# Kernel tuning notes

Measured on AMD Instinct MI355X. Metric: run time of the kernel, lower is better.

The kernel has to match this reference:

```python
import jax, jax.numpy as jnp
import numpy as np

B, N, C, E, K, L = 8, 20000, 256, 320000, 3, 2
EPS = 1e-5

def setup_inputs() -> dict:
    key = jax.random.key(0)
    ks = jax.random.split(key, 8)
    features = jax.random.normal(ks[0], (B * N, C), dtype=jnp.float32)
    edge_index = jax.random.randint(ks[1], (2, E), 0, N, dtype=jnp.int64)
    # ChebConv params per layer: K linear weights [C,C] (no per-lin bias) + one bias [C]
    W = jax.random.normal(ks[2], (L, K, C, C), dtype=jnp.float32) * 0.05
    b = jax.random.normal(ks[3], (L, C), dtype=jnp.float32) * 0.05
    # node-mode LayerNorm affine params per layer
    ln_w = jnp.ones((L, C), dtype=jnp.float32)
    ln_b = jnp.zeros((L, C), dtype=jnp.float32)
    return {"features": features, "W": W, "b": b, "ln_w": ln_w, "ln_b": ln_b,
            "edge_index": edge_index, "batch_size": B}


def reference(features, W, b, ln_w, ln_b, edge_index, batch_size):
    n = features.shape[0] // batch_size
    c = features.shape[-1]
    src, dst = edge_index[0], edge_index[1]
    # sym-normalized Laplacian, lambda_max=2: L_hat = 2L/lmax - I = -D^-1/2 A D^-1/2
    deg = jax.ops.segment_sum(jnp.ones_like(src, dtype=features.dtype), src, num_segments=n)
    dis = jnp.where(deg > 0, jax.lax.rsqrt(jnp.where(deg > 0, deg, 1.0)), 0.0)
    norm = -dis[src] * dis[dst]  # [E]
    n_layers, k_order = W.shape[0], W.shape[1]

    def prop(x):  # L_hat @ x via gather-scale-scatter
        return jax.ops.segment_sum(norm[:, None] * x[src], dst, num_segments=n)

    def cheb(x, Wl, bl):
        Tx0 = x
        out = Tx0 @ Wl[0]
        Tx1 = prop(Tx0)
        out = out + Tx1 @ Wl[1]
        for k in range(2, k_order):
            Tx2 = 2.0 * prop(Tx1) - Tx0
            out = out + Tx2 @ Wl[k]
            Tx0, Tx1 = Tx1, Tx2
        return out + bl

    def single(feats):  # [n, c] -> [n, c]
        x = feats
        for i in range(n_layers):
            # NOTE: module passes original features to every layer's conv (faithful)
            x = cheb(feats, W[i], b[i])
            mu = jnp.mean(x, axis=-1, keepdims=True)
            var = jnp.var(x, axis=-1, keepdims=True)
            x = (x - mu) * jax.lax.rsqrt(var + EPS) * ln_w[i] + ln_b[i]
            # dropout p=0.0 -> identity
        return x

    fb = features.reshape(batch_size, n, c)
    return jax.vmap(single)(fb)
```

## Files before the change

kernel.cpp:

```cpp
#include <hip/hip_runtime.h>
#include <stdint.h>

#define BB 8
#define NN 20000
#define CC 256
#define EE 320000
#define KK 3
#define MROWS (BB * NN)
#define ROWU (BB * CC)

__device__ __forceinline__ float bf2f(ushort u) {
    union { uint32_t ui; float f; } v; v.ui = ((uint32_t)u) << 16; return v.f;
}
__device__ __forceinline__ ushort f2bf(float f) {
    union { uint32_t ui; float f; } v; v.f = f;
    uint32_t r = (v.ui + 0x7FFFu + ((v.ui >> 16) & 1u)) >> 16;
    return (ushort)r;
}

typedef __bf16 bf16x8 __attribute__((ext_vector_type(8)));
typedef float  f32x4  __attribute__((ext_vector_type(4)));

__device__ __forceinline__ void gload16(const void* gptr, void* lptr) {
    __builtin_amdgcn_global_load_lds(
        (const __attribute__((address_space(1))) void*)gptr,
        (__attribute__((address_space(3))) void*)lptr, 16, 0, 0);
}

__global__ void detect_k(const int* __restrict__ raw, int* __restrict__ flag) {
    int i = blockIdx.x * 256 + threadIdx.x;
    int v = 0;
    int idx = 2 * i + 1;
    if (i < EE) v = raw[idx];
    unsigned long long m = __ballot(v != 0);
    if ((threadIdx.x & 63) == 0 && m) atomicOr(flag, 1);
}

__global__ void convert_k(const int* __restrict__ raw, const int* __restrict__ flag,
                          int* __restrict__ src, int* __restrict__ dst) {
    int e = blockIdx.x * 256 + threadIdx.x;
    if (e >= EE) return;
    if (*flag == 0) {
        src[e] = raw[2 * e];
        dst[e] = raw[2 * EE + 2 * e];
    } else {
        src[e] = raw[e];
        dst[e] = raw[EE + e];
    }
}

__global__ void count_k(const int* __restrict__ src, const int* __restrict__ dst,
                        int* __restrict__ deg_out, int* __restrict__ cnt_in) {
    int e = blockIdx.x * 256 + threadIdx.x;
    if (e >= EE) return;
    atomicAdd(&deg_out[src[e]], 1);
    atomicAdd(&cnt_in[dst[e]], 1);
}

__global__ void __launch_bounds__(1024) scan_k(const int* __restrict__ cnt_in,
                                               const int* __restrict__ deg_out,
                                               int* __restrict__ row_ptr,
                                               float* __restrict__ dis) {
    __shared__ int wpart[16];
    const int t = threadIdx.x;
    const int lane = t & 63, wid = t >> 6;
    const int base = t * 20;
    int local[20];
    int sum = 0;
#pragma unroll
    for (int i = 0; i < 20; i++) {
        int idx = base + i;
        int v = (idx < NN) ? cnt_in[idx] : 0;
        local[i] = sum;
        sum += v;
    }
    int sc = sum;
#pragma unroll
    for (int off = 1; off < 64; off <<= 1) {
        int u = __shfl_up(sc, off, 64);
        if (lane >= off) sc += u;
    }
    if (lane == 63) wpart[wid] = sc;
    __syncthreads();
    if (wid == 0 && lane < 16) {
        int v = wpart[lane];
#pragma unroll
        for (int off = 1; off < 16; off <<= 1) {
            int u = __shfl_up(v, off, 64);
            if (lane >= off) v += u;
        }
        wpart[lane] = v;
    }
    __syncthreads();
    int wbase = (wid > 0) ? wpart[wid - 1] : 0;
    int tbase = wbase + sc - sum;
#pragma unroll
    for (int i = 0; i < 20; i++) {
        int idx = base + i;
        if (idx < NN) row_ptr[idx] = tbase + local[i];
    }
    if (t == 1023) row_ptr[NN] = tbase + sum;
    for (int i = t; i < NN; i += 1024) {
        int d = deg_out[i];
        dis[i] = (d > 0) ? rsqrtf((float)d) : 0.0f;
    }
}

__global__ void fill_k(const int* __restrict__ src, const int* __restrict__ dst,
                       const int* __restrict__ row_ptr, int* __restrict__ fillc,
                       const float* __restrict__ dis,
                       int* __restrict__ col, float* __restrict__ w) {
    int e = blockIdx.x * 256 + threadIdx.x;
    if (e >= EE) return;
    int s = src[e], d = dst[e];
    int pos = row_ptr[d] + atomicAdd(&fillc[d], 1);
    col[pos] = s;
    w[pos] = -dis[s] * dis[d];
}

__global__ void cvt_k(const float* __restrict__ x, ushort* __restrict__ y) {
    size_t idx = ((size_t)blockIdx.x * 256 + threadIdx.x) * 4;
    int row = (int)(idx >> 8);
    int c = (int)(idx & 255);
    int b = row / NN, n = row - b * NN;
    float4 v = *(const float4*)(x + idx);
    ushort4 o = make_ushort4(f2bf(v.x), f2bf(v.y), f2bf(v.z), f2bf(v.w));
    *(ushort4*)(y + ((size_t)(n * BB + b) * CC + c)) = o;
}

__global__ void wprep_k(const float* __restrict__ W, ushort* __restrict__ wt) {
    int idx = blockIdx.x * 256 + threadIdx.x;
    if (idx >= 256 * 768) return;
    int n = idx / 768, k = idx % 768;
    int sel = k >> 8, kk = k & 255;
    const float* W1 = W + KK * CC * CC;
    float v;
    if (sel == 0)      v = W1[kk * CC + n] - W1[2 * CC * CC + kk * CC + n];
    else if (sel == 1) v = W1[CC * CC + kk * CC + n];
    else               v = 2.0f * W1[2 * CC * CC + kk * CC + n];
    wt[idx] = f2bf(v);
}

__global__ void __launch_bounds__(256) prop_k(const ushort* __restrict__ x,
                                              ushort* __restrict__ y,
                                              const int* __restrict__ row_ptr,
                                              const int* __restrict__ col,
                                              const float* __restrict__ w) {
    const int n = blockIdx.x;
    const int t = threadIdx.x;
    const int beg = row_ptr[n], end = row_ptr[n + 1];
    const ushort* xb = x + t * 8;
    float a0 = 0, a1 = 0, a2 = 0, a3 = 0, a4 = 0, a5 = 0, a6 = 0, a7 = 0;
    int j = beg;
    for (; j + 4 <= end; j += 4) {
        int s0 = col[j], s1 = col[j + 1], s2 = col[j + 2], s3 = col[j + 3];
        float w0 = w[j], w1 = w[j + 1], w2 = w[j + 2], w3 = w[j + 3];
        uint4 v0 = *(const uint4*)(xb + (size_t)s0 * ROWU);
        uint4 v1 = *(const uint4*)(xb + (size_t)s1 * ROWU);
        uint4 v2 = *(const uint4*)(xb + (size_t)s2 * ROWU);
        uint4 v3 = *(const uint4*)(xb + (size_t)s3 * ROWU);
        a0 += w0 * bf2f((ushort)v0.x) + w1 * bf2f((ushort)v1.x) + w2 * bf2f((ushort)v2.x) + w3 * bf2f((ushort)v3.x);
        a1 += w0 * bf2f((ushort)(v0.x >> 16)) + w1 * bf2f((ushort)(v1.x >> 16)) + w2 * bf2f((ushort)(v2.x >> 16)) + w3 * bf2f((ushort)(v3.x >> 16));
        a2 += w0 * bf2f((ushort)v0.y) + w1 * bf2f((ushort)v1.y) + w2 * bf2f((ushort)v2.y) + w3 * bf2f((ushort)v3.y);
        a3 += w0 * bf2f((ushort)(v0.y >> 16)) + w1 * bf2f((ushort)(v1.y >> 16)) + w2 * bf2f((ushort)(v2.y >> 16)) + w3 * bf2f((ushort)(v3.y >> 16));
        a4 += w0 * bf2f((ushort)v0.z) + w1 * bf2f((ushort)v1.z) + w2 * bf2f((ushort)v2.z) + w3 * bf2f((ushort)v3.z);
        a5 += w0 * bf2f((ushort)(v0.z >> 16)) + w1 * bf2f((ushort)(v1.z >> 16)) + w2 * bf2f((ushort)(v2.z >> 16)) + w3 * bf2f((ushort)(v3.z >> 16));
        a6 += w0 * bf2f((ushort)v0.w) + w1 * bf2f((ushort)v1.w) + w2 * bf2f((ushort)v2.w) + w3 * bf2f((ushort)v3.w);
        a7 += w0 * bf2f((ushort)(v0.w >> 16)) + w1 * bf2f((ushort)(v1.w >> 16)) + w2 * bf2f((ushort)(v2.w >> 16)) + w3 * bf2f((ushort)(v3.w >> 16));
    }
    for (; j < end; j++) {
        int s = col[j];
        float wt = w[j];
        uint4 v = *(const uint4*)(xb + (size_t)s * ROWU);
        a0 += wt * bf2f((ushort)v.x);
        a1 += wt * bf2f((ushort)(v.x >> 16));
        a2 += wt * bf2f((ushort)v.y);
        a3 += wt * bf2f((ushort)(v.y >> 16));
        a4 += wt * bf2f((ushort)v.z);
        a5 += wt * bf2f((ushort)(v.z >> 16));
        a6 += wt * bf2f((ushort)v.w);
        a7 += wt * bf2f((ushort)(v.w >> 16));
    }
    uint4 o;
    o.x = (uint32_t)f2bf(a0) | ((uint32_t)f2bf(a1) << 16);
    o.y = (uint32_t)f2bf(a2) | ((uint32_t)f2bf(a3) << 16);
    o.z = (uint32_t)f2bf(a4) | ((uint32_t)f2bf(a5) << 16);
    o.w = (uint32_t)f2bf(a6) | ((uint32_t)f2bf(a7) << 16);
    *(uint4*)(y + (size_t)n * ROWU + t * 8) = o;
}

__global__ void __launch_bounds__(256) gemmln_k(const ushort* __restrict__ a0,
                                                const ushort* __restrict__ a1,
                                                const ushort* __restrict__ a2,
                                                const ushort* __restrict__ wt,
                                                const float* __restrict__ bias,
                                                const float* __restrict__ lnw,
                                                const float* __restrict__ lnb,
                                                float* __restrict__ out) {
    __shared__ ushort As[64 * 32];
    __shared__ ushort Bs[256 * 32];
    __shared__ float reds[64][4];
    __shared__ float redq[64][4];
    const int tid = threadIdx.x;
    const int wid = tid >> 6, lane = tid & 63;
    const int quad = lane >> 4, l16 = lane & 15;
    const int row0 = blockIdx.x * 64;

    f32x4 acc[4][4] = {};

    for (int kt = 0; kt < 24; kt++) {
        const ushort* ab = (kt < 8) ? a0 : ((kt < 16) ? a1 : a2);
        const int kl = (kt & 7) * 32;
        const int kg = kt * 32;
        __syncthreads();
        {
            int c = wid * 64 + lane;
            int m = c >> 2, kq = (c & 3) * 8;
            gload16(ab + (size_t)(row0 + m) * CC + kl + kq, &As[(wid * 64) * 8]);
        }
#pragma unroll
        for (int q = 0; q < 4; q++) {
            int c = wid * 256 + q * 64 + lane;
            int m = c >> 2, kq = (c & 3) * 8;
            gload16(wt + (size_t)m * 768 + kg + kq, &Bs[(wid * 256 + q * 64) * 8]);
        }
        __syncthreads();

        bf16x8 af[4], bfr[4];
#pragma unroll
        for (int mt = 0; mt < 4; mt++)
            af[mt] = *(const bf16x8*)&As[(mt * 16 + l16) * 32 + quad * 8];
#pragma unroll
        for (int nt = 0; nt < 4; nt++)
            bfr[nt] = *(const bf16x8*)&Bs[(wid * 64 + nt * 16 + l16) * 32 + quad * 8];
#pragma unroll
        for (int mt = 0; mt < 4; mt++)
#pragma unroll
            for (int nt = 0; nt < 4; nt++)
                acc[mt][nt] = __builtin_amdgcn_mfma_f32_16x16x32_bf16(
                    af[mt], bfr[nt], acc[mt][nt], 0, 0, 0);
    }

    float bv[4], lwv[4], lbv[4];
#pragma unroll
    for (int nt = 0; nt < 4; nt++) {
        int c = wid * 64 + nt * 16 + l16;
        bv[nt] = bias[c]; lwv[nt] = lnw[c]; lbv[nt] = lnb[c];
    }
#pragma unroll
    for (int mt = 0; mt < 4; mt++) {
#pragma unroll
        for (int r = 0; r < 4; r++) {
            float s = 0.0f, q = 0.0f;
#pragma unroll
            for (int nt = 0; nt < 4; nt++) {
                float v = acc[mt][nt][r] + bv[nt];
                s += v; q += v * v;
            }
#pragma unroll
            for (int off = 1; off < 16; off <<= 1) {
                s += __shfl_xor(s, off, 64);
                q += __shfl_xor(q, off, 64);
            }
            if (l16 == 0) {
                int m = mt * 16 + quad * 4 + r;
                reds[m][wid] = s;
                redq[m][wid] = q;
            }
        }
    }
    __syncthreads();
#pragma unroll
    for (int mt = 0; mt < 4; mt++) {
#pragma unroll
        for (int r = 0; r < 4; r++) {
            int ml = mt * 16 + quad * 4 + r;
            float s = reds[ml][0] + reds[ml][1] + reds[ml][2] + reds[ml][3];
            float q = redq[ml][0] + redq[ml][1] + redq[ml][2] + redq[ml][3];
            float mean = s * (1.0f / CC);
            float var = q * (1.0f / CC) - mean * mean;
            float rs = rsqrtf(var + 1e-5f);
            int m = row0 + ml;
            int n = m >> 3, b = m & 7;
            size_t orow = (size_t)b * NN + n;
#pragma unroll
            for (int nt = 0; nt < 4; nt++) {
                int c = wid * 64 + nt * 16 + l16;
                float v = (acc[mt][nt][r] + bv[nt] - mean) * rs * lwv[nt] + lbv[nt];
                out[orow * CC + c] = v;
            }
        }
    }
}

extern "C" void kernel_launch(void* const* d_in, const int* in_sizes, int n_in,
                              void* d_out, int out_size, void* d_ws, size_t ws_size,
                              hipStream_t stream) {
    const float* feats = (const float*)d_in[0];
    const float* W     = (const float*)d_in[1];
    const float* bvec  = (const float*)d_in[2];
    const float* lnw   = (const float*)d_in[3];
    const float* lnb   = (const float*)d_in[4];
    const int*   eidx  = (const int*)d_in[5];
    float* outp = (float*)d_out;

    int* flag    = (int*)d_ws;
    int* deg_out = flag + 64;
    int* cnt_in  = deg_out + NN;
    int* fillc   = cnt_in + NN;
    int* row_ptr = fillc + NN;
    int* srcw    = row_ptr + (NN + 64);
    int* dstw    = srcw + EE;
    int* colw    = dstw + EE;
    float* disw  = (float*)(colw + EE);
    float* ww    = disw + (NN + 64);
    uintptr_t bf_base = ((uintptr_t)(ww + EE) + 255) & ~(uintptr_t)255;
    ushort* featsb = (ushort*)bf_base;
    ushort* tx1b   = featsb + (size_t)MROWS * CC;
    ushort* p2b    = tx1b + (size_t)MROWS * CC;
    ushort* wcat   = p2b + (size_t)MROWS * CC;

    hipMemsetAsync(flag, 0, (size_t)(64 + 3 * NN) * sizeof(int), stream);

    int eb = (EE + 255) / 256;
    detect_k<<<eb, 256, 0, stream>>>(eidx, flag);
    convert_k<<<eb, 256, 0, stream>>>(eidx, flag, srcw, dstw);
    count_k<<<eb, 256, 0, stream>>>(srcw, dstw, deg_out, cnt_in);
    scan_k<<<1, 1024, 0, stream>>>(cnt_in, deg_out, row_ptr, disw);
    fill_k<<<eb, 256, 0, stream>>>(srcw, dstw, row_ptr, fillc, disw, colw, ww);

    cvt_k<<<MROWS * CC / 1024, 256, 0, stream>>>(feats, featsb);
    wprep_k<<<(256 * 768 + 255) / 256, 256, 0, stream>>>(W, wcat);

    prop_k<<<NN, 256, 0, stream>>>(featsb, tx1b, row_ptr, colw, ww);
    prop_k<<<NN, 256, 0, stream>>>(tx1b, p2b, row_ptr, colw, ww);

    gemmln_k<<<MROWS / 64, 256, 0, stream>>>(featsb, tx1b, p2b, wcat,
                                             bvec + CC, lnw + CC, lnb + CC, outp);
}
```

Baseline: 938.3 us.

## Double GEMM row tile with 8 waves and unroll gather loop by eight

The fused GEMM+LayerNorm kernel now processes 128 rows per block with 512 threads arranged as a 2x4 wave grid. Each weight tile loaded into shared memory is therefore reused across twice as many rows, which halves weight traffic per output row. The sparse propagation kernel gains an 8-edge unrolled loop with tree-shaped sums, so more independent gathers are in flight per thread. The larger block raises register and LDS pressure per block, and the 8-way unroll adds register use in prop_k.

Result: faster. 914.5 us (-2.5%).

```diff
diff --git a/kernel.cpp b/kernel.cpp
--- a/kernel.cpp
+++ b/kernel.cpp
@@ -152,6 +152,36 @@
     const ushort* xb = x + t * 8;
     float a0 = 0, a1 = 0, a2 = 0, a3 = 0, a4 = 0, a5 = 0, a6 = 0, a7 = 0;
     int j = beg;
+    for (; j + 8 <= end; j += 8) {
+        int s0 = col[j], s1 = col[j + 1], s2 = col[j + 2], s3 = col[j + 3];
+        int s4 = col[j + 4], s5 = col[j + 5], s6 = col[j + 6], s7 = col[j + 7];
+        float w0 = w[j], w1 = w[j + 1], w2 = w[j + 2], w3 = w[j + 3];
+        float w4 = w[j + 4], w5 = w[j + 5], w6 = w[j + 6], w7 = w[j + 7];
+        uint4 v0 = *(const uint4*)(xb + (size_t)s0 * ROWU);
+        uint4 v1 = *(const uint4*)(xb + (size_t)s1 * ROWU);
+        uint4 v2 = *(const uint4*)(xb + (size_t)s2 * ROWU);
+        uint4 v3 = *(const uint4*)(xb + (size_t)s3 * ROWU);
+        uint4 v4 = *(const uint4*)(xb + (size_t)s4 * ROWU);
+        uint4 v5 = *(const uint4*)(xb + (size_t)s5 * ROWU);
+        uint4 v6 = *(const uint4*)(xb + (size_t)s6 * ROWU);
+        uint4 v7 = *(const uint4*)(xb + (size_t)s7 * ROWU);
+        a0 += ((w0 * bf2f((ushort)v0.x) + w1 * bf2f((ushort)v1.x)) + (w2 * bf2f((ushort)v2.x) + w3 * bf2f((ushort)v3.x)))
+            + ((w4 * bf2f((ushort)v4.x) + w5 * bf2f((ushort)v5.x)) + (w6 * bf2f((ushort)v6.x) + w7 * bf2f((ushort)v7.x)));
+        a1 += ((w0 * bf2f((ushort)(v0.x >> 16)) + w1 * bf2f((ushort)(v1.x >> 16))) + (w2 * bf2f((ushort)(v2.x >> 16)) + w3 * bf2f((ushort)(v3.x >> 16))))
+            + ((w4 * bf2f((ushort)(v4.x >> 16)) + w5 * bf2f((ushort)(v5.x >> 16))) + (w6 * bf2f((ushort)(v6.x >> 16)) + w7 * bf2f((ushort)(v7.x >> 16))));
+        a2 += ((w0 * bf2f((ushort)v0.y) + w1 * bf2f((ushort)v1.y)) + (w2 * bf2f((ushort)v2.y) + w3 * bf2f((ushort)v3.y)))
+            + ((w4 * bf2f((ushort)v4.y) + w5 * bf2f((ushort)v5.y)) + (w6 * bf2f((ushort)v6.y) + w7 * bf2f((ushort)v7.y)));
+        a3 += ((w0 * bf2f((ushort)(v0.y >> 16)) + w1 * bf2f((ushort)(v1.y >> 16))) + (w2 * bf2f((ushort)(v2.y >> 16)) + w3 * bf2f((ushort)(v3.y >> 16))))
+            + ((w4 * bf2f((ushort)(v4.y >> 16)) + w5 * bf2f((ushort)(v5.y >> 16))) + (w6 * bf2f((ushort)(v6.y >> 16)) + w7 * bf2f((ushort)(v7.y >> 16))));
+        a4 += ((w0 * bf2f((ushort)v0.z) + w1 * bf2f((ushort)v1.z)) + (w2 * bf2f((ushort)v2.z) + w3 * bf2f((ushort)v3.z)))
+            + ((w4 * bf2f((ushort)v4.z) + w5 * bf2f((ushort)v5.z)) + (w6 * bf2f((ushort)v6.z) + w7 * bf2f((ushort)v7.z)));
+        a5 += ((w0 * bf2f((ushort)(v0.z >> 16)) + w1 * bf2f((ushort)(v1.z >> 16))) + (w2 * bf2f((ushort)(v2.z >> 16)) + w3 * bf2f((ushort)(v3.z >> 16))))
+            + ((w4 * bf2f((ushort)(v4.z >> 16)) + w5 * bf2f((ushort)(v5.z >> 16))) + (w6 * bf2f((ushort)(v6.z >> 16)) + w7 * bf2f((ushort)(v7.z >> 16))));
+        a6 += ((w0 * bf2f((ushort)v0.w) + w1 * bf2f((ushort)v1.w)) + (w2 * bf2f((ushort)v2.w) + w3 * bf2f((ushort)v3.w)))
+            + ((w4 * bf2f((ushort)v4.w) + w5 * bf2f((ushort)v5.w)) + (w6 * bf2f((ushort)v6.w) + w7 * bf2f((ushort)v7.w)));
+        a7 += ((w0 * bf2f((ushort)(v0.w >> 16)) + w1 * bf2f((ushort)(v1.w >> 16))) + (w2 * bf2f((ushort)(v2.w >> 16)) + w3 * bf2f((ushort)(v3.w >> 16))))
+            + ((w4 * bf2f((ushort)(v4.w >> 16)) + w5 * bf2f((ushort)(v5.w >> 16))) + (w6 * bf2f((ushort)(v6.w >> 16)) + w7 * bf2f((ushort)(v7.w >> 16))));
+    }
     for (; j + 4 <= end; j += 4) {
         int s0 = col[j], s1 = col[j + 1], s2 = col[j + 2], s3 = col[j + 3];
         float w0 = w[j], w1 = w[j + 1], w2 = w[j + 2], w3 = w[j + 3];
@@ -159,14 +189,14 @@
         uint4 v1 = *(const uint4*)(xb + (size_t)s1 * ROWU);
         uint4 v2 = *(const uint4*)(xb + (size_t)s2 * ROWU);
         uint4 v3 = *(const uint4*)(xb + (size_t)s3 * ROWU);
-        a0 += w0 * bf2f((ushort)v0.x) + w1 * bf2f((ushort)v1.x) + w2 * bf2f((ushort)v2.x) + w3 * bf2f((ushort)v3.x);
-        a1 += w0 * bf2f((ushort)(v0.x >> 16)) + w1 * bf2f((ushort)(v1.x >> 16)) + w2 * bf2f((ushort)(v2.x >> 16)) + w3 * bf2f((ushort)(v3.x >> 16));
-        a2 += w0 * bf2f((ushort)v0.y) + w1 * bf2f((ushort)v1.y) + w2 * bf2f((ushort)v2.y) + w3 * bf2f((ushort)v3.y);
-        a3 += w0 * bf2f((ushort)(v0.y >> 16)) + w1 * bf2f((ushort)(v1.y >> 16)) + w2 * bf2f((ushort)(v2.y >> 16)) + w3 * bf2f((ushort)(v3.y >> 16));
-        a4 += w0 * bf2f((ushort)v0.z) + w1 * bf2f((ushort)v1.z) + w2 * bf2f((ushort)v2.z) + w3 * bf2f((ushort)v3.z);
-        a5 += w0 * bf2f((ushort)(v0.z >> 16)) + w1 * bf2f((ushort)(v1.z >> 16)) + w2 * bf2f((ushort)(v2.z >> 16)) + w3 * bf2f((ushort)(v3.z >> 16));
-        a6 += w0 * bf2f((ushort)v0.w) + w1 * bf2f((ushort)v1.w) + w2 * bf2f((ushort)v2.w) + w3 * bf2f((ushort)v3.w);
-        a7 += w0 * bf2f((ushort)(v0.w >> 16)) + w1 * bf2f((ushort)(v1.w >> 16)) + w2 * bf2f((ushort)(v2.w >> 16)) + w3 * bf2f((ushort)(v3.w >> 16));
+        a0 += (w0 * bf2f((ushort)v0.x) + w1 * bf2f((ushort)v1.x)) + (w2 * bf2f((ushort)v2.x) + w3 * bf2f((ushort)v3.x));
+        a1 += (w0 * bf2f((ushort)(v0.x >> 16)) + w1 * bf2f((ushort)(v1.x >> 16))) + (w2 * bf2f((ushort)(v2.x >> 16)) + w3 * bf2f((ushort)(v3.x >> 16)));
+        a2 += (w0 * bf2f((ushort)v0.y) + w1 * bf2f((ushort)v1.y)) + (w2 * bf2f((ushort)v2.y) + w3 * bf2f((ushort)v3.y));
+        a3 += (w0 * bf2f((ushort)(v0.y >> 16)) + w1 * bf2f((ushort)(v1.y >> 16))) + (w2 * bf2f((ushort)(v2.y >> 16)) + w3 * bf2f((ushort)(v3.y >> 16)));
+        a4 += (w0 * bf2f((ushort)v0.z) + w1 * bf2f((ushort)v1.z)) + (w2 * bf2f((ushort)v2.z) + w3 * bf2f((ushort)v3.z));
+        a5 += (w0 * bf2f((ushort)(v0.z >> 16)) + w1 * bf2f((ushort)(v1.z >> 16))) + (w2 * bf2f((ushort)(v2.z >> 16)) + w3 * bf2f((ushort)(v3.z >> 16)));
+        a6 += (w0 * bf2f((ushort)v0.w) + w1 * bf2f((ushort)v1.w)) + (w2 * bf2f((ushort)v2.w) + w3 * bf2f((ushort)v3.w));
+        a7 += (w0 * bf2f((ushort)(v0.w >> 16)) + w1 * bf2f((ushort)(v1.w >> 16))) + (w2 * bf2f((ushort)(v2.w >> 16)) + w3 * bf2f((ushort)(v3.w >> 16)));
     }
     for (; j < end; j++) {
         int s = col[j];
@@ -189,22 +219,23 @@
     *(uint4*)(y + (size_t)n * ROWU + t * 8) = o;
 }
 
-__global__ void __launch_bounds__(256) gemmln_k(const ushort* __restrict__ a0,
-                                                const ushort* __restrict__ a1,
-                                                const ushort* __restrict__ a2,
-                                                const ushort* __restrict__ wt,
-                                                const float* __restrict__ bias,
-                                                const float* __restrict__ lnw,
-                                                const float* __restrict__ lnb,
-                                                float* __restrict__ out) {
-    __shared__ ushort As[64 * 32];
+__global__ void __launch_bounds__(512, 4) gemmln_k(const ushort* __restrict__ a0,
+                                                   const ushort* __restrict__ a1,
+                                                   const ushort* __restrict__ a2,
+                                                   const ushort* __restrict__ wt,
+                                                   const float* __restrict__ bias,
+                                                   const float* __restrict__ lnw,
+                                                   const float* __restrict__ lnb,
+                                                   float* __restrict__ out) {
+    __shared__ ushort As[128 * 32];
     __shared__ ushort Bs[256 * 32];
-    __shared__ float reds[64][4];
-    __shared__ float redq[64][4];
+    __shared__ float reds[128][4];
+    __shared__ float redq[128][4];
     const int tid = threadIdx.x;
     const int wid = tid >> 6, lane = tid & 63;
+    const int wrow = wid >> 2, wcol = wid & 3;
     const int quad = lane >> 4, l16 = lane & 15;
-    const int row0 = blockIdx.x * 64;
+    const int row0 = blockIdx.x * 128;
 
     f32x4 acc[4][4] = {};
 
@@ -214,25 +245,24 @@
         const int kg = kt * 32;
         __syncthreads();
         {
-            int c = wid * 64 + lane;
+            int m = tid >> 2, kq = (tid & 3) * 8;
+            gload16(ab + (size_t)(row0 + m) * CC + kl + kq, &As[(wid * 64) * 8]);
+        }
+#pragma unroll
+        for (int q = 0; q < 2; q++) {
+            int c = q * 512 + tid;
             int m = c >> 2, kq = (c & 3) * 8;
-            gload16(ab + (size_t)(row0 + m) * CC + kl + kq, &As[(wid * 64) * 8]);
-        }
-#pragma unroll
-        for (int q = 0; q < 4; q++) {
-            int c = wid * 256 + q * 64 + lane;
-            int m = c >> 2, kq = (c & 3) * 8;
-            gload16(wt + (size_t)m * 768 + kg + kq, &Bs[(wid * 256 + q * 64) * 8]);
+            gload16(wt + (size_t)m * 768 + kg + kq, &Bs[(q * 512 + wid * 64) * 8]);
         }
         __syncthreads();
 
         bf16x8 af[4], bfr[4];
 #pragma unroll
         for (int mt = 0; mt < 4; mt++)
-            af[mt] = *(const bf16x8*)&As[(mt * 16 + l16) * 32 + quad * 8];
+            af[mt] = *(const bf16x8*)&As[(wrow * 64 + mt * 16 + l16) * 32 + quad * 8];
 #pragma unroll
         for (int nt = 0; nt < 4; nt++)
-            bfr[nt] = *(const bf16x8*)&Bs[(wid * 64 + nt * 16 + l16) * 32 + quad * 8];
+            bfr[nt] = *(const bf16x8*)&Bs[(wcol * 64 + nt * 16 + l16) * 32 + quad * 8];
 #pragma unroll
         for (int mt = 0; mt < 4; mt++)
 #pragma unroll
@@ -244,7 +274,7 @@
     float bv[4], lwv[4], lbv[4];
 #pragma unroll
     for (int nt = 0; nt < 4; nt++) {
-        int c = wid * 64 + nt * 16 + l16;
+        int c = wcol * 64 + nt * 16 + l16;
         bv[nt] = bias[c]; lwv[nt] = lnw[c]; lbv[nt] = lnb[c];
     }
 #pragma unroll
@@ -263,9 +293,9 @@
                 q += __shfl_xor(q, off, 64);
             }
             if (l16 == 0) {
-                int m = mt * 16 + quad * 4 + r;
-                reds[m][wid] = s;
-                redq[m][wid] = q;
+                int ml = wrow * 64 + mt * 16 + quad * 4 + r;
+                reds[ml][wcol] = s;
+                redq[ml][wcol] = q;
             }
         }
     }
@@ -274,7 +304,7 @@
     for (int mt = 0; mt < 4; mt++) {
 #pragma unroll
         for (int r = 0; r < 4; r++) {
-            int ml = mt * 16 + quad * 4 + r;
+            int ml = wrow * 64 + mt * 16 + quad * 4 + r;
             float s = reds[ml][0] + reds[ml][1] + reds[ml][2] + reds[ml][3];
             float q = redq[ml][0] + redq[ml][1] + redq[ml][2] + redq[ml][3];
             float mean = s * (1.0f / CC);
@@ -285,7 +315,7 @@
             size_t orow = (size_t)b * NN + n;
 #pragma unroll
             for (int nt = 0; nt < 4; nt++) {
-                int c = wid * 64 + nt * 16 + l16;
+                int c = wcol * 64 + nt * 16 + l16;
                 float v = (acc[mt][nt][r] + bv[nt] - mean) * rs * lwv[nt] + lbv[nt];
                 out[orow * CC + c] = v;
             }
@@ -335,6 +365,6 @@
     prop_k<<<NN, 256, 0, stream>>>(featsb, tx1b, row_ptr, colw, ww);
     prop_k<<<NN, 256, 0, stream>>>(tx1b, p2b, row_ptr, colw, ww);
 
-    gemmln_k<<<MROWS / 64, 256, 0, stream>>>(featsb, tx1b, p2b, wcat,
-                                             bvec + CC, lnw + CC, lnb + CC, outp);
-}
+    gemmln_k<<<MROWS / 128, 512, 0, stream>>>(featsb, tx1b, p2b, wcat,
+                                              bvec + CC, lnw + CC, lnb + CC, outp);
+}
```
